# Optimization experiments

Hardware: AMD Instinct MI355X
Metric: run time of the kernel (lower is better)

Reference implementation:

```python
import jax, jax.numpy as jnp
import numpy as np

B, L_IMG, L_TXT, DM, H, D = 1, 4096, 512, 3072, 24, 128
EPS = 1e-6


def _rms(x, scale):
    # flax nnx RMSNorm: x * rsqrt(mean(x^2) + eps) * scale
    var = jnp.mean(jnp.square(x), axis=-1, keepdims=True)
    return x * jax.lax.rsqrt(var + EPS) * scale


def _qkv(x, W, qn, kn):
    b, l = x.shape[:2]
    qkv = (x @ W).reshape(b, l, 3, H, D).transpose(2, 0, 3, 1, 4)  # [3,B,H,L,D]
    q, k, v = qkv[0], qkv[1], qkv[2]
    return _rms(q, qn), _rms(k, kn), v


def setup_inputs() -> dict:
    key = jax.random.key(0)
    ks = jax.random.split(key, 8)
    s = 0.02
    return {
        "hidden_states": jax.random.normal(ks[0], (B, L_IMG, DM), jnp.float32),
        "encoder_hidden_states": jax.random.normal(ks[1], (B, L_TXT, DM), jnp.float32),
        "image_rotary_emb": jax.random.normal(ks[2], (L_TXT + L_IMG, D // 2, 4), jnp.float32),
        "W_iqkv": jax.random.normal(ks[3], (DM, 3 * H * D), jnp.float32) * s,
        "W_eqkv": jax.random.normal(ks[4], (DM, 3 * H * D), jnp.float32) * s,
        "W_iproj": jax.random.normal(ks[5], (H * D, DM), jnp.float32) * s,
        "b_iproj": jnp.zeros((DM,), jnp.float32),
        "W_eproj": jax.random.normal(ks[6], (H * D, DM), jnp.float32) * s,
        "b_eproj": jnp.zeros((DM,), jnp.float32),
        "qn_scale": jnp.ones((D,), jnp.float32),
        "kn_scale": jnp.ones((D,), jnp.float32),
        "eqn_scale": jnp.ones((D,), jnp.float32),
        "ekn_scale": jnp.ones((D,), jnp.float32),
    }


def reference(hidden_states, encoder_hidden_states, image_rotary_emb,
              W_iqkv, W_eqkv, W_iproj, b_iproj, W_eproj, b_eproj,
              qn_scale, kn_scale, eqn_scale, ekn_scale):
    scale = D ** -0.5
    l_txt = encoder_hidden_states.shape[1]

    q, k, v = _qkv(hidden_states, W_iqkv, qn_scale, kn_scale)           # [B,H,L_img,D]
    eq, ek, ev = _qkv(encoder_hidden_states, W_eqkv, eqn_scale, ekn_scale)

    q = jnp.concatenate((eq, q), axis=2)   # [B,H,L,D], L = L_txt + L_img
    k = jnp.concatenate((ek, k), axis=2)
    v = jnp.concatenate((ev, v), axis=2)

    # RoPE: freqs_cis [L, D/2, 2, 2]
    fc = image_rotary_emb.reshape(image_rotary_emb.shape[0], image_rotary_emb.shape[1], 2, 2)

    def rope(x):
        x_ = x.reshape(*x.shape[:-1], -1, 1, 2)  # [B,H,L,D/2,1,2]
        out = fc[..., 0] * x_[..., 0] + fc[..., 1] * x_[..., 1]  # [B,H,L,D/2,2]
        return out.reshape(*x.shape).astype(x.dtype)

    q, k = rope(q), rope(k)

    # flatten heads into feature dim BEFORE attention (faithful to original)
    def merge(x):
        b, h, l, d = x.shape
        return x.transpose(0, 2, 1, 3).reshape(b, l, h * d)

    qm, km, vm = merge(q), merge(k), merge(v)  # [B,L,H*D]

    attn = jax.nn.softmax(jnp.einsum('bqd,bkd->bqk', qm, km) * scale, axis=-1)
    out = jnp.einsum('bqk,bkd->bqd', attn, vm)  # [B,L,H*D]

    ctx_out, img_out = out[:, :l_txt], out[:, l_txt:]
    img_out = img_out @ W_iproj + b_iproj
    ctx_out = ctx_out @ W_eproj + b_eproj
    return img_out, ctx_out
```

## Files before the change

kernel.cpp:

```cpp
#include <hip/hip_runtime.h>
#include <hip/hip_bf16.h>
#include <cstdint>

typedef __attribute__((ext_vector_type(8))) short u16x8;
typedef _Float16 f16_t;
typedef __attribute__((ext_vector_type(8))) f16_t f16x8;
typedef __attribute__((ext_vector_type(4))) float f32x4;

#define L_TOT 4608
#define L_TXT 512
#define L_IMG 4096
#define NH 24
#define HD 128
#define DMODEL 3072
#define NQKV 9216
#define LOG2E 1.44269504088896340736f
#define S_SHIFT 32.0f

__device__ __forceinline__ ushort f2h(float f) {
  union { f16_t h; ushort u; } c; c.h = (f16_t)f; return c.u;
}
__device__ __forceinline__ float h2f(ushort u) {
  union { ushort u; f16_t h; } c; c.u = u; return (float)c.h;
}
__device__ __forceinline__ void gload16(const ushort* g, ushort* l) {
  __builtin_amdgcn_global_load_lds((const __attribute__((address_space(1))) void*)g,
                                   (__attribute__((address_space(3))) void*)l, 16, 0, 0);
}

__global__ void cvt_f32_f16(const float* __restrict__ src, ushort* __restrict__ dst,
                            int n8) {
  const int i = blockIdx.x * 256 + threadIdx.x;
  if (i >= n8) return;
  const f32x4 a = *(const f32x4*)(src + (size_t)i * 8);
  const f32x4 b = *(const f32x4*)(src + (size_t)i * 8 + 4);
  alignas(16) ushort o[8];
#pragma unroll
  for (int j = 0; j < 4; ++j) { o[j] = f2h(a[j]); o[4 + j] = f2h(b[j]); }
  *(u16x8*)(dst + (size_t)i * 8) = *(const u16x8*)o;
}

__global__ void tconv_w(const float* __restrict__ src, int C, int c0,
                        ushort* __restrict__ dst) {
  __shared__ ushort tile[64][72];
  const int nb = blockIdx.x << 6, kb = blockIdx.y << 6;
  const int t = threadIdx.x;
  const int lr = t >> 2, lc = (t & 3) << 4;
  const float* sp = src + (size_t)(kb + lr) * C + c0 + nb + lc;
  const f32x4 v0 = *(const f32x4*)sp;
  const f32x4 v1 = *(const f32x4*)(sp + 4);
  const f32x4 v2 = *(const f32x4*)(sp + 8);
  const f32x4 v3 = *(const f32x4*)(sp + 12);
#pragma unroll
  for (int i = 0; i < 4; ++i) {
    tile[lr][lc + i]      = f2h(v0[i]);
    tile[lr][lc + 4 + i]  = f2h(v1[i]);
    tile[lr][lc + 8 + i]  = f2h(v2[i]);
    tile[lr][lc + 12 + i] = f2h(v3[i]);
  }
  __syncthreads();
  const int cl = t & 63, rb = (t >> 6) << 4;
  alignas(16) ushort o[16];
#pragma unroll
  for (int i = 0; i < 16; ++i) o[i] = tile[rb + i][cl];
  ushort* dp = dst + (size_t)(nb + cl) * DMODEL + kb + rb;
  *(u16x8*)dp       = *(const u16x8*)o;
  *(u16x8*)(dp + 8) = *(const u16x8*)(o + 8);
}

__global__ void tconv_h(const ushort* __restrict__ src, ushort* __restrict__ dst,
                        int R, int C) {
  __shared__ ushort tile[64][72];
  const int r0 = blockIdx.y << 6, c0 = blockIdx.x << 6;
  const int t = threadIdx.x;
  const int lr = t >> 2, lc = (t & 3) << 4;
  const ushort* sp = src + (size_t)(r0 + lr) * C + c0 + lc;
  const u16x8 v0 = *(const u16x8*)sp;
  const u16x8 v1 = *(const u16x8*)(sp + 8);
#pragma unroll
  for (int i = 0; i < 8; ++i) {
    tile[lr][lc + i]     = ((const ushort*)&v0)[i];
    tile[lr][lc + 8 + i] = ((const ushort*)&v1)[i];
  }
  __syncthreads();
  const int cl = t & 63, rb = (t >> 6) << 4;
  alignas(16) ushort o[16];
#pragma unroll
  for (int i = 0; i < 16; ++i) o[i] = tile[rb + i][cl];
  ushort* dp = dst + (size_t)(c0 + cl) * R + r0 + rb;
  *(u16x8*)dp       = *(const u16x8*)o;
  *(u16x8*)(dp + 8) = *(const u16x8*)(o + 8);
}

template <int MODE>
__global__ __launch_bounds__(512, 2) void gemm256(
    const ushort* __restrict__ A, int lda, const ushort* __restrict__ Bt, int ldb,
    int M, int N, int K, void* __restrict__ out0, ushort* __restrict__ out1,
    ushort* __restrict__ out2, const float* __restrict__ bias, int l_off, int n_base) {
  __shared__ __align__(16) ushort lds[2][2][2][8192];
  int lin = blockIdx.y * gridDim.x + blockIdx.x;
  {
    const int nwg = gridDim.x * gridDim.y;
    const int q8 = nwg >> 3, r8 = nwg & 7;
    const int xcd = lin & 7, idx = lin >> 3;
    lin = (xcd < r8 ? xcd * (q8 + 1) : r8 * (q8 + 1) + (xcd - r8) * q8) + idx;
  }
  const int m0 = (lin % gridDim.x) << 8, n0 = (lin / gridDim.x) << 8;
  const int tid = threadIdx.x, w = tid >> 6, lane = tid & 63;
  const int wm = w >> 2, wn = w & 3;
  const int lr = lane & 15, g4 = lane >> 4;
  const int srow = lane >> 2;
  const int soff = 8 * ((lane & 3) ^ ((lane >> 3) & 3));
  f32x4 acc[8][4];
#pragma unroll
  for (int a = 0; a < 8; ++a)
#pragma unroll
    for (int b = 0; b < 4; ++b) acc[a][b] = (f32x4){0.f, 0.f, 0.f, 0.f};
  const int nt = K >> 6;

  auto stageA = [&](int h, int kt, int b) {
#pragma unroll
    for (int i = 0; i < 2; ++i) {
      const int j = w * 2 + i;
      gload16(A + (size_t)(m0 + 16 * j + srow) * lda + (kt << 6) + 32 * h + soff,
              &lds[b][h][0][j * 512]);
    }
  };
  auto stageB = [&](int h, int kt, int b) {
#pragma unroll
    for (int i = 0; i < 2; ++i) {
      const int j = w * 2 + i;
      gload16(Bt + (size_t)(n0 + 16 * j + srow) * ldb + (kt << 6) + 32 * h + soff,
              &lds[b][h][1][j * 512]);
    }
  };
  auto readA = [&](int h, int mi, int b) -> f16x8 {
    const int row = wm * 128 + mi * 16 + lr;
    const int byte = row * 64 + ((g4 ^ ((row >> 1) & 3)) << 4);
    return *(const f16x8*)((const char*)&lds[b][h][0][0] + byte);
  };
  auto readB = [&](int h, int ni, int b) -> f16x8 {
    const int row = wn * 64 + ni * 16 + lr;
    const int byte = row * 64 + ((g4 ^ ((row >> 1) & 3)) << 4);
    return *(const f16x8*)((const char*)&lds[b][h][1][0] + byte);
  };

  stageA(0, 0, 0); stageB(0, 0, 0); stageA(1, 0, 0); stageB(1, 0, 0);

  for (int kt = 0; kt < nt; ++kt) {
    const int c = kt & 1, sb = c ^ 1;
    const int st = (kt + 1 < nt) ? kt + 1 : 0;
    f16x8 bf[4], af[8];
    asm volatile("s_waitcnt vmcnt(4)" ::: "memory");
    asm volatile("s_barrier" ::: "memory");
    stageA(0, st, sb); stageB(0, st, sb);
#pragma unroll
    for (int ni = 0; ni < 4; ++ni) bf[ni] = readB(0, ni, c);
#pragma unroll
    for (int m = 0; m < 8; ++m) af[m] = readA(0, m, c);
    __builtin_amdgcn_s_setprio(1);
#pragma unroll
    for (int m = 0; m < 8; ++m)
#pragma unroll
      for (int ni = 0; ni < 4; ++ni)
        acc[m][ni] = __builtin_amdgcn_mfma_f32_16x16x32_f16(af[m], bf[ni], acc[m][ni], 0, 0, 0);
    __builtin_amdgcn_s_setprio(0);
    asm volatile("s_waitcnt vmcnt(4)" ::: "memory");
    asm volatile("s_barrier" ::: "memory");
    stageA(1, st, sb); stageB(1, st, sb);
#pragma unroll
    for (int ni = 0; ni < 4; ++ni) bf[ni] = readB(1, ni, c);
#pragma unroll
    for (int m = 0; m < 8; ++m) af[m] = readA(1, m, c);
    __builtin_amdgcn_s_setprio(1);
#pragma unroll
    for (int m = 0; m < 8; ++m)
#pragma unroll
      for (int ni = 0; ni < 4; ++ni)
        acc[m][ni] = __builtin_amdgcn_mfma_f32_16x16x32_f16(af[m], bf[ni], acc[m][ni], 0, 0, 0);
    __builtin_amdgcn_s_setprio(0);
  }

  const int rb = (lane >> 4) << 2;
  const int cl = lane & 15;
  if (MODE == 0) {
    const int g = n_base + n0;
    const int which = g / DMODEL;
    const int col0 = g - which * DMODEL;
    ushort* dst = (which == 0) ? (ushort*)out0 : (which == 1) ? out1 : out2;
#pragma unroll
    for (int mi = 0; mi < 8; ++mi)
#pragma unroll
      for (int j = 0; j < 4; ++j) {
        const int l = l_off + m0 + wm * 128 + mi * 16 + rb + j;
        const size_t rbase = (size_t)l * DMODEL + col0 + wn * 64 + cl;
#pragma unroll
        for (int ni = 0; ni < 4; ++ni) dst[rbase + ni * 16] = f2h(acc[mi][ni][j]);
      }
  } else if (MODE == 1) {
    float* outf = (float*)out0;
    float bv[4];
#pragma unroll
    for (int ni = 0; ni < 4; ++ni) bv[ni] = bias[n0 + wn * 64 + ni * 16 + cl];
#pragma unroll
    for (int mi = 0; mi < 8; ++mi)
#pragma unroll
      for (int j = 0; j < 4; ++j) {
        const int r = m0 + wm * 128 + mi * 16 + rb + j;
        const size_t rbase = (size_t)r * N + n0 + wn * 64 + cl;
#pragma unroll
        for (int ni = 0; ni < 4; ++ni) outf[rbase + ni * 16] = acc[mi][ni][j] + bv[ni];
      }
  } else {
    ushort* outb = (ushort*)out0;
    const float sh = (MODE == 3) ? S_SHIFT : 0.0f;
#pragma unroll
    for (int mi = 0; mi < 8; ++mi)
#pragma unroll
      for (int j = 0; j < 4; ++j) {
        const int r = m0 + wm * 128 + mi * 16 + rb + j;
        const size_t rbase = (size_t)r * N + n0 + wn * 64 + cl;
#pragma unroll
        for (int ni = 0; ni < 4; ++ni) outb[rbase + ni * 16] = f2h(acc[mi][ni][j] - sh);
      }
  }
}

template <int MODE>
__global__ void gemm128(const ushort* __restrict__ A, int lda,
                        const ushort* __restrict__ Bt, int ldb,
                        int M, int N, int K, void* __restrict__ out0,
                        ushort* __restrict__ out1, ushort* __restrict__ out2,
                        const float* __restrict__ bias, int l_off, int n_base) {
  __shared__ __align__(16) ushort Alds[128 * 32];
  __shared__ __align__(16) ushort Blds[128 * 32];
  const int m0 = blockIdx.x << 7, n0 = blockIdx.y << 7;
  const int tid = threadIdx.x, wave = tid >> 6, lane = tid & 63;
  const int wr = wave >> 1, wc = wave & 1;
  const int lrow = lane & 15, lk8 = (lane >> 4) << 3;
  f32x4 acc[4][4];
#pragma unroll
  for (int a = 0; a < 4; ++a)
#pragma unroll
    for (int b = 0; b < 4; ++b) acc[a][b] = (f32x4){0.f, 0.f, 0.f, 0.f};
  const int nk = K >> 5;
  const ushort* Ap = A + (size_t)(m0 + (tid >> 2)) * lda + ((tid & 3) << 3);
  const ushort* Bp = Bt + (size_t)(n0 + (tid >> 2)) * ldb + ((tid & 3) << 3);
  for (int ks = 0; ks < nk; ++ks) {
    __syncthreads();
    const ushort* a0 = Ap + (ks << 5);
    gload16(a0, &Alds[wave << 9]);
    gload16(a0 + (size_t)64 * lda, &Alds[2048 + (wave << 9)]);
    const ushort* b0 = Bp + (ks << 5);
    gload16(b0, &Blds[wave << 9]);
    gload16(b0 + (size_t)64 * ldb, &Blds[2048 + (wave << 9)]);
    __syncthreads();
    f16x8 af[4], bfr[4];
#pragma unroll
    for (int mt = 0; mt < 4; ++mt)
      af[mt] = *(const f16x8*)&Alds[((wr << 6) + (mt << 4) + lrow) * 32 + lk8];
#pragma unroll
    for (int nt = 0; nt < 4; ++nt)
      bfr[nt] = *(const f16x8*)&Blds[((wc << 6) + (nt << 4) + lrow) * 32 + lk8];
#pragma unroll
    for (int mt = 0; mt < 4; ++mt)
#pragma unroll
      for (int nt = 0; nt < 4; ++nt)
        acc[mt][nt] = __builtin_amdgcn_mfma_f32_16x16x32_f16(af[mt], bfr[nt], acc[mt][nt], 0, 0, 0);
  }
  const int rb = (lane >> 4) << 2;
  if (MODE == 0) {
    const int g = n_base + n0;
    const int which = g / DMODEL;
    const int col0 = g - which * DMODEL;
    ushort* dst = (which == 0) ? (ushort*)out0 : (which == 1) ? out1 : out2;
#pragma unroll
    for (int mt = 0; mt < 4; ++mt)
#pragma unroll
      for (int j = 0; j < 4; ++j) {
        const int l = l_off + m0 + (wr << 6) + (mt << 4) + rb + j;
        const size_t rbase = (size_t)l * DMODEL + col0 + (wc << 6) + lrow;
#pragma unroll
        for (int nt = 0; nt < 4; ++nt) dst[rbase + (nt << 4)] = f2h(acc[mt][nt][j]);
      }
  } else {
    float* outf = (float*)out0;
    float bv[4];
#pragma unroll
    for (int nt = 0; nt < 4; ++nt) bv[nt] = bias[n0 + (wc << 6) + (nt << 4) + lrow];
#pragma unroll
    for (int mt = 0; mt < 4; ++mt)
#pragma unroll
      for (int j = 0; j < 4; ++j) {
        const int r = m0 + (wr << 6) + (mt << 4) + rb + j;
        const size_t rbase = (size_t)r * N + n0 + (wc << 6) + lrow;
#pragma unroll
        for (int nt = 0; nt < 4; ++nt) outf[rbase + (nt << 4)] = acc[mt][nt][j] + bv[nt];
      }
  }
}

__global__ void norm_rope(ushort* __restrict__ Q, ushort* __restrict__ Kg,
                          const float* __restrict__ rope,
                          const float* __restrict__ qn, const float* __restrict__ kn,
                          const float* __restrict__ eqn, const float* __restrict__ ekn) {
  const int idx = (blockIdx.x << 2) + (threadIdx.x >> 6);
  const int lane = threadIdx.x & 63;
  const int h = idx % NH, l = idx / NH;
  const float* qsc = (l < L_TXT) ? eqn : qn;
  const float* ksc = (l < L_TXT) ? ekn : kn;
  const size_t base = (size_t)l * DMODEL + h * HD + (lane << 1);
  const f32x4 fcv = *(const f32x4*)(rope + ((size_t)l * 64 + lane) * 4);
  const float fa = fcv[0], fb = fcv[1], fc = fcv[2], fd = fcv[3];
  const float s0 = qsc[lane << 1], s1 = qsc[(lane << 1) + 1];
  const float t0 = ksc[lane << 1], t1 = ksc[(lane << 1) + 1];
  {
    const uint32_t qv = *(const uint32_t*)&Q[base];
    float x0 = h2f((ushort)(qv & 0xffff)), x1 = h2f((ushort)(qv >> 16));
    float ss = x0 * x0 + x1 * x1;
#pragma unroll
    for (int m = 1; m < 64; m <<= 1) ss += __shfl_xor(ss, m);
    const float r = rsqrtf(ss * (1.0f / 128.0f) + 1e-6f);
    x0 *= r * s0;
    x1 *= r * s1;
    const float o0 = (fa * x0 + fb * x1) * 0.08838834764831845f;
    const float o1 = (fc * x0 + fd * x1) * 0.08838834764831845f;
    *(uint32_t*)&Q[base] = (uint32_t)f2h(o0) | ((uint32_t)f2h(o1) << 16);
  }
  {
    const uint32_t kv = *(const uint32_t*)&Kg[base];
    float x0 = h2f((ushort)(kv & 0xffff)), x1 = h2f((ushort)(kv >> 16));
    float ss = x0 * x0 + x1 * x1;
#pragma unroll
    for (int m = 1; m < 64; m <<= 1) ss += __shfl_xor(ss, m);
    const float r = rsqrtf(ss * (1.0f / 128.0f) + 1e-6f);
    x0 *= r * t0;
    x1 *= r * t1;
    const float o0 = fa * x0 + fb * x1;
    const float o1 = fc * x0 + fd * x1;
    *(uint32_t*)&Kg[base] = (uint32_t)f2h(o0) | ((uint32_t)f2h(o1) << 16);
  }
}

__global__ void softmax_rows(ushort* __restrict__ S) {
  const int r = blockIdx.x, tid = threadIdx.x;
  ushort* Sr = S + (size_t)r * L_TOT;
  float v[18];
  float m = -3.0e38f;
#pragma unroll
  for (int j = 0; j < 18; ++j) { v[j] = h2f(Sr[tid + (j << 8)]); m = fmaxf(m, v[j]); }
#pragma unroll
  for (int o = 1; o < 64; o <<= 1) m = fmaxf(m, __shfl_xor(m, o));
  __shared__ float redm[4], reds[4];
  const int wave = tid >> 6, lane = tid & 63;
  if (lane == 0) redm[wave] = m;
  __syncthreads();
  m = fmaxf(fmaxf(redm[0], redm[1]), fmaxf(redm[2], redm[3]));
  float s = 0.f;
#pragma unroll
  for (int j = 0; j < 18; ++j) { v[j] = exp2f((v[j] - m) * LOG2E); s += v[j]; }
#pragma unroll
  for (int o = 1; o < 64; o <<= 1) s += __shfl_xor(s, o);
  if (lane == 0) reds[wave] = s;
  __syncthreads();
  const float inv = 1.0f / (reds[0] + reds[1] + reds[2] + reds[3]);
#pragma unroll
  for (int j = 0; j < 18; ++j) Sr[tid + (j << 8)] = f2h(v[j] * inv);
}

extern "C" void kernel_launch(void* const* d_in, const int* in_sizes, int n_in,
                              void* d_out, int out_size, void* d_ws, size_t ws_size,
                              hipStream_t stream) {
  (void)in_sizes; (void)n_in; (void)out_size; (void)ws_size;
  const float* hidden  = (const float*)d_in[0];
  const float* enc     = (const float*)d_in[1];
  const float* rope    = (const float*)d_in[2];
  const float* W_iqkv  = (const float*)d_in[3];
  const float* W_eqkv  = (const float*)d_in[4];
  const float* W_iproj = (const float*)d_in[5];
  const float* b_iproj = (const float*)d_in[6];
  const float* W_eproj = (const float*)d_in[7];
  const float* b_eproj = (const float*)d_in[8];
  const float* qn  = (const float*)d_in[9];
  const float* kn  = (const float*)d_in[10];
  const float* eqn = (const float*)d_in[11];
  const float* ekn = (const float*)d_in[12];
  float* out = (float*)d_out;

  const size_t SZ_S  = (size_t)L_TOT * L_TOT;
  const size_t SZ_LD = (size_t)L_TOT * DMODEL;
  ushort* R0  = (ushort*)d_ws;
  ushort* CF  = R0;
  ushort* S   = R0;
  ushort* QR  = R0 + SZ_S;
  ushort* KR  = QR + SZ_LD;
  ushort* VR  = KR + SZ_LD;
  ushort* VT  = KR;
  ushort* AO  = QR;
  ushort* WP  = VR;
  ushort* WTD = (ushort*)out;

  dim3 blk(256);
  cvt_f32_f16<<<dim3(L_TXT * DMODEL / 8 / 256), blk, 0, stream>>>(enc, CF,
                                                                  L_TXT * DMODEL / 8);
  cvt_f32_f16<<<dim3(L_IMG * DMODEL / 8 / 256), blk, 0, stream>>>(
      hidden, CF + (size_t)L_TXT * DMODEL, L_IMG * DMODEL / 8);
  tconv_w<<<dim3(NQKV / 64, DMODEL / 64), blk, 0, stream>>>(W_iqkv, NQKV, 0, WTD);
  gemm256<0><<<dim3(L_IMG / 256, NQKV / 256), dim3(512), 0, stream>>>(
      CF + (size_t)L_TXT * DMODEL, DMODEL, WTD, DMODEL, L_IMG, NQKV, DMODEL,
      QR, KR, VR, nullptr, L_TXT, 0);
  tconv_w<<<dim3(NQKV / 64, DMODEL / 64), blk, 0, stream>>>(W_eqkv, NQKV, 0, WTD);
  gemm128<0><<<dim3(L_TXT / 128, NQKV / 128), blk, 0, stream>>>(
      CF, DMODEL, WTD, DMODEL, L_TXT, NQKV, DMODEL, QR, KR, VR, nullptr, 0, 0);
  norm_rope<<<dim3(L_TOT * NH / 4), blk, 0, stream>>>(QR, KR, rope, qn, kn, eqn, ekn);
  gemm256<3><<<dim3(L_TOT / 256, L_TOT / 256), dim3(512), 0, stream>>>(
      QR, DMODEL, KR, DMODEL, L_TOT, L_TOT, DMODEL, S, nullptr, nullptr, nullptr, 0, 0);
  softmax_rows<<<dim3(L_TOT), blk, 0, stream>>>(S);
  tconv_h<<<dim3(48, 72), blk, 0, stream>>>(VR, VT, L_TOT, DMODEL);
  gemm256<2><<<dim3(L_TOT / 256, DMODEL / 256), dim3(512), 0, stream>>>(
      S, L_TOT, VT, L_TOT, L_TOT, DMODEL, L_TOT, AO, nullptr, nullptr, nullptr, 0, 0);
  tconv_w<<<dim3(48, 48), blk, 0, stream>>>(W_iproj, DMODEL, 0, WP);
  gemm256<1><<<dim3(L_IMG / 256, DMODEL / 256), dim3(512), 0, stream>>>(
      AO + (size_t)L_TXT * DMODEL, DMODEL, WP, DMODEL, L_IMG, DMODEL, DMODEL,
      out, nullptr, nullptr, b_iproj, 0, 0);
  tconv_w<<<dim3(48, 48), blk, 0, stream>>>(W_eproj, DMODEL, 0, WP);
  gemm128<1><<<dim3(L_TXT / 128, DMODEL / 128), blk, 0, stream>>>(
      AO, DMODEL, WP, DMODEL, L_TXT, DMODEL, DMODEL,
      out + (size_t)L_IMG * DMODEL, nullptr, nullptr, b_eproj, 0, 0);
}
```

Before: 933.5 us.

## Merge text and image QKV/projection GEMMs into single 256-tile launches with per-tile weight selection

```diff
diff --git a/kernel.cpp b/kernel.cpp
--- a/kernel.cpp
+++ b/kernel.cpp
@@ -94,9 +94,11 @@
 
 template <int MODE>
 __global__ __launch_bounds__(512, 2) void gemm256(
-    const ushort* __restrict__ A, int lda, const ushort* __restrict__ Bt, int ldb,
-    int M, int N, int K, void* __restrict__ out0, ushort* __restrict__ out1,
-    ushort* __restrict__ out2, const float* __restrict__ bias, int l_off, int n_base) {
+    const ushort* __restrict__ A, int lda,
+    const ushort* __restrict__ BtLo, const ushort* __restrict__ BtHi, int ldb,
+    int N, int K, void* __restrict__ out0, ushort* __restrict__ out1,
+    ushort* __restrict__ out2, const float* __restrict__ biasLo,
+    const float* __restrict__ biasHi, int n_base) {
   __shared__ __align__(16) ushort lds[2][2][2][8192];
   int lin = blockIdx.y * gridDim.x + blockIdx.x;
   {
@@ -106,6 +108,7 @@
     lin = (xcd < r8 ? xcd * (q8 + 1) : r8 * (q8 + 1) + (xcd - r8) * q8) + idx;
   }
   const int m0 = (lin % gridDim.x) << 8, n0 = (lin / gridDim.x) << 8;
+  const ushort* Bt = (m0 < L_TXT) ? BtLo : BtHi;
   const int tid = threadIdx.x, w = tid >> 6, lane = tid & 63;
   const int wm = w >> 2, wn = w & 3;
   const int lr = lane & 15, g4 = lane >> 4;
@@ -192,13 +195,15 @@
     for (int mi = 0; mi < 8; ++mi)
 #pragma unroll
       for (int j = 0; j < 4; ++j) {
-        const int l = l_off + m0 + wm * 128 + mi * 16 + rb + j;
+        const int l = m0 + wm * 128 + mi * 16 + rb + j;
         const size_t rbase = (size_t)l * DMODEL + col0 + wn * 64 + cl;
 #pragma unroll
         for (int ni = 0; ni < 4; ++ni) dst[rbase + ni * 16] = f2h(acc[mi][ni][j]);
       }
   } else if (MODE == 1) {
     float* outf = (float*)out0;
+    const float* bias = (m0 < L_TXT) ? biasLo : biasHi;
+    const int rofs = (m0 < L_TXT) ? L_IMG : -L_TXT;
     float bv[4];
 #pragma unroll
     for (int ni = 0; ni < 4; ++ni) bv[ni] = bias[n0 + wn * 64 + ni * 16 + cl];
@@ -206,7 +211,7 @@
     for (int mi = 0; mi < 8; ++mi)
 #pragma unroll
       for (int j = 0; j < 4; ++j) {
-        const int r = m0 + wm * 128 + mi * 16 + rb + j;
+        const int r = m0 + wm * 128 + mi * 16 + rb + j + rofs;
         const size_t rbase = (size_t)r * N + n0 + wn * 64 + cl;
 #pragma unroll
         for (int ni = 0; ni < 4; ++ni) outf[rbase + ni * 16] = acc[mi][ni][j] + bv[ni];
@@ -222,80 +227,6 @@
         const size_t rbase = (size_t)r * N + n0 + wn * 64 + cl;
 #pragma unroll
         for (int ni = 0; ni < 4; ++ni) outb[rbase + ni * 16] = f2h(acc[mi][ni][j] - sh);
-      }
-  }
-}
-
-template <int MODE>
-__global__ void gemm128(const ushort* __restrict__ A, int lda,
-                        const ushort* __restrict__ Bt, int ldb,
-                        int M, int N, int K, void* __restrict__ out0,
-                        ushort* __restrict__ out1, ushort* __restrict__ out2,
-                        const float* __restrict__ bias, int l_off, int n_base) {
-  __shared__ __align__(16) ushort Alds[128 * 32];
-  __shared__ __align__(16) ushort Blds[128 * 32];
-  const int m0 = blockIdx.x << 7, n0 = blockIdx.y << 7;
-  const int tid = threadIdx.x, wave = tid >> 6, lane = tid & 63;
-  const int wr = wave >> 1, wc = wave & 1;
-  const int lrow = lane & 15, lk8 = (lane >> 4) << 3;
-  f32x4 acc[4][4];
-#pragma unroll
-  for (int a = 0; a < 4; ++a)
-#pragma unroll
-    for (int b = 0; b < 4; ++b) acc[a][b] = (f32x4){0.f, 0.f, 0.f, 0.f};
-  const int nk = K >> 5;
-  const ushort* Ap = A + (size_t)(m0 + (tid >> 2)) * lda + ((tid & 3) << 3);
-  const ushort* Bp = Bt + (size_t)(n0 + (tid >> 2)) * ldb + ((tid & 3) << 3);
-  for (int ks = 0; ks < nk; ++ks) {
-    __syncthreads();
-    const ushort* a0 = Ap + (ks << 5);
-    gload16(a0, &Alds[wave << 9]);
-    gload16(a0 + (size_t)64 * lda, &Alds[2048 + (wave << 9)]);
-    const ushort* b0 = Bp + (ks << 5);
-    gload16(b0, &Blds[wave << 9]);
-    gload16(b0 + (size_t)64 * ldb, &Blds[2048 + (wave << 9)]);
-    __syncthreads();
-    f16x8 af[4], bfr[4];
-#pragma unroll
-    for (int mt = 0; mt < 4; ++mt)
-      af[mt] = *(const f16x8*)&Alds[((wr << 6) + (mt << 4) + lrow) * 32 + lk8];
-#pragma unroll
-    for (int nt = 0; nt < 4; ++nt)
-      bfr[nt] = *(const f16x8*)&Blds[((wc << 6) + (nt << 4) + lrow) * 32 + lk8];
-#pragma unroll
-    for (int mt = 0; mt < 4; ++mt)
-#pragma unroll
-      for (int nt = 0; nt < 4; ++nt)
-        acc[mt][nt] = __builtin_amdgcn_mfma_f32_16x16x32_f16(af[mt], bfr[nt], acc[mt][nt], 0, 0, 0);
-  }
-  const int rb = (lane >> 4) << 2;
-  if (MODE == 0) {
-    const int g = n_base + n0;
-    const int which = g / DMODEL;
-    const int col0 = g - which * DMODEL;
-    ushort* dst = (which == 0) ? (ushort*)out0 : (which == 1) ? out1 : out2;
-#pragma unroll
-    for (int mt = 0; mt < 4; ++mt)
-#pragma unroll
-      for (int j = 0; j < 4; ++j) {
-        const int l = l_off + m0 + (wr << 6) + (mt << 4) + rb + j;
-        const size_t rbase = (size_t)l * DMODEL + col0 + (wc << 6) + lrow;
-#pragma unroll
-        for (int nt = 0; nt < 4; ++nt) dst[rbase + (nt << 4)] = f2h(acc[mt][nt][j]);
-      }
-  } else {
-    float* outf = (float*)out0;
-    float bv[4];
-#pragma unroll
-    for (int nt = 0; nt < 4; ++nt) bv[nt] = bias[n0 + (wc << 6) + (nt << 4) + lrow];
-#pragma unroll
-    for (int mt = 0; mt < 4; ++mt)
-#pragma unroll
-      for (int j = 0; j < 4; ++j) {
-        const int r = m0 + (wr << 6) + (mt << 4) + rb + j;
-        const size_t rbase = (size_t)r * N + n0 + (wc << 6) + lrow;
-#pragma unroll
-        for (int nt = 0; nt < 4; ++nt) outf[rbase + (nt << 4)] = acc[mt][nt][j] + bv[nt];
       }
   }
 }
@@ -389,6 +320,7 @@
 
   const size_t SZ_S  = (size_t)L_TOT * L_TOT;
   const size_t SZ_LD = (size_t)L_TOT * DMODEL;
+  const size_t SZ_WH = (size_t)L_TOT * DMODEL;
   ushort* R0  = (ushort*)d_ws;
   ushort* CF  = R0;
   ushort* S   = R0;
@@ -397,34 +329,36 @@
   ushort* VR  = KR + SZ_LD;
   ushort* VT  = KR;
   ushort* AO  = QR;
-  ushort* WP  = VR;
-  ushort* WTD = (ushort*)out;
+  ushort* WTe = (ushort*)out;
+  ushort* WTi = WTe + SZ_WH;
+  ushort* WPi = R0;
+  ushort* WPe = R0 + (size_t)DMODEL * DMODEL;
 
   dim3 blk(256);
   cvt_f32_f16<<<dim3(L_TXT * DMODEL / 8 / 256), blk, 0, stream>>>(enc, CF,
                                                                   L_TXT * DMODEL / 8);
   cvt_f32_f16<<<dim3(L_IMG * DMODEL / 8 / 256), blk, 0, stream>>>(
       hidden, CF + (size_t)L_TXT * DMODEL, L_IMG * DMODEL / 8);
-  tconv_w<<<dim3(NQKV / 64, DMODEL / 64), blk, 0, stream>>>(W_iqkv, NQKV, 0, WTD);
-  gemm256<0><<<dim3(L_IMG / 256, NQKV / 256), dim3(512), 0, stream>>>(
-      CF + (size_t)L_TXT * DMODEL, DMODEL, WTD, DMODEL, L_IMG, NQKV, DMODEL,
-      QR, KR, VR, nullptr, L_TXT, 0);
-  tconv_w<<<dim3(NQKV / 64, DMODEL / 64), blk, 0, stream>>>(W_eqkv, NQKV, 0, WTD);
-  gemm128<0><<<dim3(L_TXT / 128, NQKV / 128), blk, 0, stream>>>(
-      CF, DMODEL, WTD, DMODEL, L_TXT, NQKV, DMODEL, QR, KR, VR, nullptr, 0, 0);
+  for (int h = 0; h < 2; ++h) {
+    const int c0 = h * 4608;
+    tconv_w<<<dim3(72, 48), blk, 0, stream>>>(W_eqkv, NQKV, c0, WTe);
+    tconv_w<<<dim3(72, 48), blk, 0, stream>>>(W_iqkv, NQKV, c0, WTi);
+    gemm256<0><<<dim3(L_TOT / 256, 18), dim3(512), 0, stream>>>(
+        CF, DMODEL, WTe, WTi, DMODEL, 4608, DMODEL,
+        QR, KR, VR, nullptr, nullptr, c0);
+  }
   norm_rope<<<dim3(L_TOT * NH / 4), blk, 0, stream>>>(QR, KR, rope, qn, kn, eqn, ekn);
   gemm256<3><<<dim3(L_TOT / 256, L_TOT / 256), dim3(512), 0, stream>>>(
-      QR, DMODEL, KR, DMODEL, L_TOT, L_TOT, DMODEL, S, nullptr, nullptr, nullptr, 0, 0);
+      QR, DMODEL, KR, KR, DMODEL, L_TOT, DMODEL, S, nullptr, nullptr,
+      nullptr, nullptr, 0);
   softmax_rows<<<dim3(L_TOT), blk, 0, stream>>>(S);
   tconv_h<<<dim3(48, 72), blk, 0, stream>>>(VR, VT, L_TOT, DMODEL);
   gemm256<2><<<dim3(L_TOT / 256, DMODEL / 256), dim3(512), 0, stream>>>(
-      S, L_TOT, VT, L_TOT, L_TOT, DMODEL, L_TOT, AO, nullptr, nullptr, nullptr, 0, 0);
-  tconv_w<<<dim3(48, 48), blk, 0, stream>>>(W_iproj, DMODEL, 0, WP);
-  gemm256<1><<<dim3(L_IMG / 256, DMODEL / 256), dim3(512), 0, stream>>>(
-      AO + (size_t)L_TXT * DMODEL, DMODEL, WP, DMODEL, L_IMG, DMODEL, DMODEL,
-      out, nullptr, nullptr, b_iproj, 0, 0);
-  tconv_w<<<dim3(48, 48), blk, 0, stream>>>(W_eproj, DMODEL, 0, WP);
-  gemm128<1><<<dim3(L_TXT / 128, DMODEL / 128), blk, 0, stream>>>(
-      AO, DMODEL, WP, DMODEL, L_TXT, DMODEL, DMODEL,
-      out + (size_t)L_IMG * DMODEL, nullptr, nullptr, b_eproj, 0, 0);
-}
+      S, L_TOT, VT, VT, L_TOT, DMODEL, L_TOT, AO, nullptr, nullptr,
+      nullptr, nullptr, 0);
+  tconv_w<<<dim3(48, 48), blk, 0, stream>>>(W_iproj, DMODEL, 0, WPi);
+  tconv_w<<<dim3(48, 48), blk, 0, stream>>>(W_eproj, DMODEL, 0, WPe);
+  gemm256<1><<<dim3(L_TOT / 256, DMODEL / 256), dim3(512), 0, stream>>>(
+      AO, DMODEL, WPe, WPi, DMODEL, DMODEL, DMODEL,
+      out, nullptr, nullptr, b_eproj, b_iproj, 0);
+}
```

Result: faster. 877.1 us (-6.0%).
